# Kernel tuning notes

Measured on AMD Instinct MI355X. Metric: run time of the kernel, lower is better.

## Reference

```python
import jax, jax.numpy as jnp
import numpy as np
from jax import lax

MEM_SLOTS = 100
DECAY = 0.9


def setup_inputs() -> dict:
    key = jax.random.key(0)
    k1, k2, k3 = jax.random.split(key, 3)
    feats = jax.random.normal(k1, (32, 512, 64, 64), dtype=jnp.float32)
    preds = jax.random.uniform(k2, (32, 1, 64, 64), dtype=jnp.float32)
    W = jax.random.normal(k3, (256, 512), dtype=jnp.float32) * 0.02
    b = jnp.zeros((256,), dtype=jnp.float32)
    return {"feats": feats, "preds": preds, "W": W, "b": b, "epoch": 20}


def _update_memory(pooled, threshold):
    """Sequential codebook update: cosine-sim match -> EMA update or append.
    pooled: [B, C]. Returns (memory [100, C], ptr int32)."""
    C = pooled.shape[1]
    slot_ids = jnp.arange(MEM_SLOTS)

    def step(carry, x):
        memory, ptr = carry
        xn = x / jnp.linalg.norm(x)
        norms = jnp.linalg.norm(memory, axis=-1, keepdims=True)
        mem_n = memory / jnp.where(norms == 0, 1.0, norms)
        sims = mem_n @ xn                                   # [100]
        sims = jnp.where(slot_ids < ptr, sims, -jnp.inf)
        idx = jnp.argmax(sims)
        val = sims[idx]
        do_ema = (ptr > 0) & (val >= threshold)
        ema_mem = memory.at[idx].set(memory[idx] * DECAY + (1.0 - DECAY) * x)
        app_mem = memory.at[ptr].set(x)
        new_mem = jnp.where(do_ema, ema_mem, app_mem)
        new_ptr = jnp.where(do_ema, ptr, ptr + 1)
        return (new_mem, new_ptr), None

    init = (jnp.zeros((MEM_SLOTS, C), pooled.dtype), jnp.int32(0))
    (memory, ptr), _ = lax.scan(step, init, pooled)
    return memory, ptr


def reference(feats, preds, W, b, epoch):
    # 1x1 conv projection 512 -> 256
    proj = jnp.einsum('oc,bchw->bohw', W, feats) + b[None, :, None, None]
    B, C, H, Wd = proj.shape
    HW = H * Wd

    # dynamic threshold (epoch % 10 == 0 in original schedule)
    threshold = (epoch / 10 - 2) * 0.4 / 13 + 0.3

    # masked average pooling (no-grad path in original)
    pooled = jnp.mean(lax.stop_gradient(proj).reshape(B, C, HW)
                      * preds.reshape(B, 1, HW), axis=-1)   # [B, C]
    memory, ptr = _update_memory(pooled, threshold)
    memory = lax.stop_gradient(memory)                      # buffer, no grad

    # memory cross-attention over valid slots only
    key_ = proj.reshape(B, C, HW)
    logit = jnp.einsum('pc,bcl->bpl', memory, key_)         # [B, 100, HW]
    valid = (jnp.arange(MEM_SLOTS) < ptr)[None, :, None]
    logit = jnp.where(valid, logit, -jnp.inf)
    attn = jax.nn.softmax(logit, axis=1)                    # softmax over slots
    aug = jnp.einsum('bpl,pc->bcl', attn, memory).reshape(B, C, H, Wd)
    return jnp.concatenate([proj, aug], axis=1)             # [B, 512, H, W]
```

## Files before the change

### kernel.cpp

```cpp
#include <hip/hip_runtime.h>
#include <math.h>

#define CH_IN   512
#define CH_OUT  256
#define HWD     4096
#define BATCH   32
#define MAXSLOT 32

typedef __attribute__((ext_vector_type(8))) short short8;
typedef __attribute__((ext_vector_type(4))) float floatx4;

__device__ __forceinline__ unsigned int pk_bf16(float a, float b) {
    unsigned int ua = __float_as_uint(a);
    ua += 0x7fffu + ((ua >> 16) & 1u);
    unsigned int ub = __float_as_uint(b);
    ub += 0x7fffu + ((ub >> 16) & 1u);
    return (ua >> 16) | (ub & 0xffff0000u);
}

#define PA 40
#define PB 42
__global__ __launch_bounds__(256) void k1_proj_gemm(
    const float* __restrict__ feats, const float* __restrict__ preds,
    const float* __restrict__ W, const float* __restrict__ bias,
    float* __restrict__ out, float* __restrict__ pooled)
{
    __shared__ __align__(16) unsigned short As[128 * PA];
    __shared__ __align__(16) unsigned short Bs[128 * PB];

    const int t  = threadIdx.x;
    const int bid  = blockIdx.x;
    const int xcd  = bid & 7;
    const int slot = bid >> 3;
    const int tile = xcd * 128 + (slot >> 1);
    const int ot   = slot & 1;
    const int lt   = tile & 31;
    const int b    = tile >> 5;

    const int l0 = lt * 128, o0 = ot * 128;
    const int lane = t & 63, wid = t >> 6;
    const int wm = wid & 1, wn = wid >> 1;
    const int ln = lane & 15, quad = lane >> 4;

    floatx4 acc[4][4];
    #pragma unroll
    for (int i = 0; i < 4; i++)
        #pragma unroll
        for (int j = 0; j < 4; j++) acc[i][j] = (floatx4){0.f, 0.f, 0.f, 0.f};

    const float* Wb = W + (size_t)o0 * CH_IN;
    const float* Fb = feats + (size_t)b * CH_IN * HWD + l0;

    const int oA = t >> 3, c4 = t & 7;
    const int l4 = t & 31;
    const int cg = t >> 5;

    float4 wst[4], fst[4];
    #pragma unroll
    for (int q = 0; q < 4; q++)
        wst[q] = *(const float4*)(Wb + (size_t)(oA + 32 * q) * CH_IN + c4 * 4);
    #pragma unroll
    for (int j = 0; j < 4; j++)
        fst[j] = *(const float4*)(Fb + (size_t)(cg * 4 + j) * HWD + l4 * 4);

    #pragma unroll 1
    for (int k0 = 0; k0 < CH_IN; k0 += 32) {
        #pragma unroll
        for (int q = 0; q < 4; q++) {
            unsigned int u0 = pk_bf16(wst[q].x, wst[q].y);
            unsigned int u1 = pk_bf16(wst[q].z, wst[q].w);
            *(uint2*)(As + (oA + 32 * q) * PA + c4 * 4) = make_uint2(u0, u1);
        }
        {
            const float v0[4] = {fst[0].x, fst[0].y, fst[0].z, fst[0].w};
            const float v1[4] = {fst[1].x, fst[1].y, fst[1].z, fst[1].w};
            const float v2[4] = {fst[2].x, fst[2].y, fst[2].z, fst[2].w};
            const float v3[4] = {fst[3].x, fst[3].y, fst[3].z, fst[3].w};
            #pragma unroll
            for (int i = 0; i < 4; i++) {
                unsigned short* row = Bs + (l4 * 4 + i) * PB + cg * 4;
                *(unsigned int*)(row)     = pk_bf16(v0[i], v1[i]);
                *(unsigned int*)(row + 2) = pk_bf16(v2[i], v3[i]);
            }
        }
        __syncthreads();

        if (k0 + 32 < CH_IN) {
            #pragma unroll
            for (int q = 0; q < 4; q++)
                wst[q] = *(const float4*)(Wb + (size_t)(oA + 32 * q) * CH_IN
                                          + (k0 + 32) + c4 * 4);
            #pragma unroll
            for (int j = 0; j < 4; j++)
                fst[j] = *(const float4*)(Fb + (size_t)(k0 + 32 + cg * 4 + j) * HWD
                                          + l4 * 4);
        }

        short8 af[4], bf[4];
        #pragma unroll
        for (int mt = 0; mt < 4; mt++) {
            int row = wm * 64 + mt * 16 + ln;
            af[mt] = *(const short8*)(As + row * PA + quad * 8);
        }
        #pragma unroll
        for (int nt = 0; nt < 4; nt++) {
            int row = wn * 64 + nt * 16 + ln;
            const unsigned short* p = Bs + row * PB + quad * 8;
            union { short8 v; unsigned int u[4]; } r;
            r.u[0] = *(const unsigned int*)(p);
            r.u[1] = *(const unsigned int*)(p + 2);
            r.u[2] = *(const unsigned int*)(p + 4);
            r.u[3] = *(const unsigned int*)(p + 6);
            bf[nt] = r.v;
        }
        #pragma unroll
        for (int mt = 0; mt < 4; mt++)
            #pragma unroll
            for (int nt = 0; nt < 4; nt++)
                acc[mt][nt] = __builtin_amdgcn_mfma_f32_16x16x32_bf16(
                    af[mt], bf[nt], acc[mt][nt], 0, 0, 0);
        __syncthreads();
    }

    float pv[4];
    #pragma unroll
    for (int nt = 0; nt < 4; nt++)
        pv[nt] = preds[(size_t)b * HWD + l0 + wn * 64 + nt * 16 + ln];

    #pragma unroll
    for (int mt = 0; mt < 4; mt++) {
        #pragma unroll
        for (int r = 0; r < 4; r++) {
            int o = o0 + wm * 64 + mt * 16 + quad * 4 + r;
            float bv = bias[o];
            float* op = out + ((size_t)b * 512 + o) * HWD + l0 + wn * 64;
            float psum = 0.f;
            #pragma unroll
            for (int nt = 0; nt < 4; nt++) {
                float val = acc[mt][nt][r] + bv;
                op[nt * 16 + ln] = val;
                psum += val * pv[nt];
            }
            #pragma unroll
            for (int off = 1; off < 16; off <<= 1)
                psum += __shfl_xor(psum, off, 64);
            if (ln == 0)
                atomicAdd(&pooled[(size_t)b * CH_OUT + o], psum);
        }
    }
}

__global__ __launch_bounds__(1024) void k2_mem_update(
    const float* __restrict__ pooled, const int* __restrict__ epoch_p,
    float* __restrict__ mem_out, int* __restrict__ ptr_out)
{
    __shared__ float mem[MAXSLOT][256];
    __shared__ float xs[256];
    __shared__ float norms2[MAXSLOT];
    __shared__ float sims[MAXSLOT];
    __shared__ float red[4];
    __shared__ float xnorm2_s;
    __shared__ int ptr_s, row_s, ema_s;

    const int t = threadIdx.x;
    const int lane = t & 63, wid = t >> 6;

    if (t < 256)
        for (int r = 0; r < MAXSLOT; r++) mem[r][t] = 0.f;
    if (t < MAXSLOT) norms2[t] = 0.f;
    if (t == 0) ptr_s = 0;

    double thr_d = ((double)(*epoch_p)) / 10.0 - 2.0;
    thr_d = thr_d * 0.4 / 13.0 + 0.3;
    const float thr = (float)thr_d;
    __syncthreads();

    for (int bi = 0; bi < BATCH; bi++) {
        if (t < 256) {
            float x = pooled[(size_t)bi * 256 + t] * (1.0f / 4096.0f);
            xs[t] = x;
            float s = x * x;
            #pragma unroll
            for (int off = 32; off >= 1; off >>= 1) s += __shfl_xor(s, off, 64);
            if (lane == 0) red[wid] = s;
        }
        __syncthreads();
        if (t == 0) xnorm2_s = red[0] + red[1] + red[2] + red[3];
        __syncthreads();

        const int P = ptr_s;
        const float xn = sqrtf(xnorm2_s);
        for (int p = wid; p < P; p += 16) {
            float d = mem[p][lane]       * xs[lane]
                    + mem[p][lane + 64]  * xs[lane + 64]
                    + mem[p][lane + 128] * xs[lane + 128]
                    + mem[p][lane + 192] * xs[lane + 192];
            #pragma unroll
            for (int off = 32; off >= 1; off >>= 1) d += __shfl_xor(d, off, 64);
            if (lane == 0) {
                float nrm = sqrtf(norms2[p]);
                if (nrm == 0.f) nrm = 1.f;
                sims[p] = d / (nrm * xn);
            }
        }
        __syncthreads();

        if (wid == 0) {
            float v = (lane < P) ? sims[lane] : -INFINITY;
            int idx = lane;
            #pragma unroll
            for (int off = 32; off >= 1; off >>= 1) {
                float ov = __shfl_down(v, off, 64);
                int   oi = __shfl_down(idx, off, 64);
                if (ov > v || (ov == v && oi < idx)) { v = ov; idx = oi; }
            }
            if (lane == 0) {
                int ema = (P > 0 && v >= thr) ? 1 : 0;
                ema_s = ema;
                row_s = ema ? idx : P;
                if (!ema) ptr_s = P + 1;
            }
        }
        __syncthreads();

        const int r = row_s;
        if (t < 256) {
            float nv = ema_s ? (mem[r][t] * 0.9f + 0.1f * xs[t]) : xs[t];
            mem[r][t] = nv;
            float s2 = nv * nv;
            #pragma unroll
            for (int off = 32; off >= 1; off >>= 1) s2 += __shfl_xor(s2, off, 64);
            if (lane == 0) red[wid] = s2;
        }
        __syncthreads();
        if (t == 0) norms2[r] = red[0] + red[1] + red[2] + red[3];
        __syncthreads();
    }

    if (t < 256)
        for (int r = 0; r < MAXSLOT; r++) mem_out[(size_t)r * 256 + t] = mem[r][t];
    if (t == 0) ptr_out[0] = ptr_s;
}

#define PT  132
#define PMS 40
#define PBS 42
__global__ __launch_bounds__(256) void k3_attention(
    const float* __restrict__ mem_g, const int* __restrict__ ptr_g,
    float* __restrict__ out)
{
    __shared__ __align__(16) unsigned short memS[10240];
    __shared__ __align__(16) unsigned short Bs[128 * PBS];
    __shared__ __align__(16) float attnL[MAXSLOT * PT];

    const int t = threadIdx.x;
    const int lt = blockIdx.x, b = blockIdx.y;
    const int l0 = lt * 128;
    const int P = ptr_g[0];

    const int lane = t & 63, wid = t >> 6;
    const int wm = wid & 1, wn = wid >> 1;
    const int ln = lane & 15, quad = lane >> 4;

    #pragma unroll
    for (int q = 0; q < 16; q++) {
        int idx = t + 256 * q;
        int p = idx >> 7, cp = idx & 127;
        float2 v = *(const float2*)(mem_g + (size_t)p * 256 + cp * 2);
        *(unsigned int*)(memS + (cp >> 4) * (32 * PMS) + p * PMS + (cp & 15) * 2)
            = pk_bf16(v.x, v.y);
    }

    const float* Pb = out + (size_t)b * 512 * HWD + l0;
    const int l4 = t & 31;
    const int cg = t >> 5;

    floatx4 accA[4];
    #pragma unroll
    for (int nt = 0; nt < 4; nt++) accA[nt] = (floatx4){0.f, 0.f, 0.f, 0.f};

    for (int k0 = 0; k0 < 8; k0++) {
        float4 f0 = *(const float4*)(Pb + (size_t)(k0 * 32 + cg * 4 + 0) * HWD + l4 * 4);
        float4 f1 = *(const float4*)(Pb + (size_t)(k0 * 32 + cg * 4 + 1) * HWD + l4 * 4);
        float4 f2 = *(const float4*)(Pb + (size_t)(k0 * 32 + cg * 4 + 2) * HWD + l4 * 4);
        float4 f3 = *(const float4*)(Pb + (size_t)(k0 * 32 + cg * 4 + 3) * HWD + l4 * 4);
        {
            const float v0[4] = {f0.x, f0.y, f0.z, f0.w};
            const float v1[4] = {f1.x, f1.y, f1.z, f1.w};
            const float v2[4] = {f2.x, f2.y, f2.z, f2.w};
            const float v3[4] = {f3.x, f3.y, f3.z, f3.w};
            #pragma unroll
            for (int i = 0; i < 4; i++) {
                unsigned short* row = Bs + (l4 * 4 + i) * PBS + cg * 4;
                *(unsigned int*)(row)     = pk_bf16(v0[i], v1[i]);
                *(unsigned int*)(row + 2) = pk_bf16(v2[i], v3[i]);
            }
        }
        __syncthreads();

        short8 af = *(const short8*)(memS + k0 * (32 * PMS) + (wm * 16 + ln) * PMS + quad * 8);
        short8 bf[4];
        #pragma unroll
        for (int nt = 0; nt < 4; nt++) {
            const unsigned short* p = Bs + (wn * 64 + nt * 16 + ln) * PBS + quad * 8;
            union { short8 v; unsigned int u[4]; } r;
            r.u[0] = *(const unsigned int*)(p);
            r.u[1] = *(const unsigned int*)(p + 2);
            r.u[2] = *(const unsigned int*)(p + 4);
            r.u[3] = *(const unsigned int*)(p + 6);
            bf[nt] = r.v;
        }
        #pragma unroll
        for (int nt = 0; nt < 4; nt++)
            accA[nt] = __builtin_amdgcn_mfma_f32_16x16x32_bf16(af, bf[nt], accA[nt], 0, 0, 0);
        __syncthreads();
    }

    #pragma unroll
    for (int nt = 0; nt < 4; nt++)
        #pragma unroll
        for (int r = 0; r < 4; r++)
            attnL[(wm * 16 + quad * 4 + r) * PT + wn * 64 + nt * 16 + ln] = accA[nt][r];
    __syncthreads();

    if (t < 128) {
        float m = -INFINITY;
        for (int p = 0; p < P; p++) m = fmaxf(m, attnL[p * PT + t]);
        float d = 0.f;
        for (int p = 0; p < P; p++) {
            float e = __expf(attnL[p * PT + t] - m);
            attnL[p * PT + t] = e;
            d += e;
        }
        float inv = 1.f / d;
        for (int p = 0; p < P; p++) attnL[p * PT + t] *= inv;
    }
    __syncthreads();

    if (t < 128) {
        #pragma unroll
        for (int pp = 0; pp < 16; pp++) {
            float a = (2 * pp     < P) ? attnL[(2 * pp) * PT + t]     : 0.f;
            float c = (2 * pp + 1 < P) ? attnL[(2 * pp + 1) * PT + t] : 0.f;
            *(unsigned int*)(Bs + t * PBS + pp * 2) = pk_bf16(a, c);
        }
    }
    #pragma unroll
    for (int q = 0; q < 16; q++) {
        int idx = t + 256 * q;
        int c = idx & 255, pp = idx >> 8;
        float va = mem_g[(size_t)(2 * pp)     * 256 + c];
        float vb = mem_g[(size_t)(2 * pp + 1) * 256 + c];
        *(unsigned int*)(memS + c * PMS + pp * 2) = pk_bf16(va, vb);
    }
    __syncthreads();

    short8 bfc[4];
    #pragma unroll
    for (int nt = 0; nt < 4; nt++) {
        const unsigned short* p = Bs + (wn * 64 + nt * 16 + ln) * PBS + quad * 8;
        union { short8 v; unsigned int u[4]; } r;
        r.u[0] = *(const unsigned int*)(p);
        r.u[1] = *(const unsigned int*)(p + 2);
        r.u[2] = *(const unsigned int*)(p + 4);
        r.u[3] = *(const unsigned int*)(p + 6);
        bfc[nt] = r.v;
    }
    const floatx4 zf = (floatx4){0.f, 0.f, 0.f, 0.f};
    for (int h = 0; h < 2; h++) {
        const int cbase = h * 128 + wm * 64;
        short8 afc[4];
        #pragma unroll
        for (int ct = 0; ct < 4; ct++)
            afc[ct] = *(const short8*)(memS + (cbase + ct * 16 + ln) * PMS + quad * 8);
        #pragma unroll
        for (int ct = 0; ct < 4; ct++) {
            floatx4 accC[4];
            #pragma unroll
            for (int nt = 0; nt < 4; nt++)
                accC[nt] = __builtin_amdgcn_mfma_f32_16x16x32_bf16(afc[ct], bfc[nt], zf, 0, 0, 0);
            #pragma unroll
            for (int r = 0; r < 4; r++) {
                int c = cbase + ct * 16 + quad * 4 + r;
                float* op = out + ((size_t)b * 512 + 256 + c) * HWD + l0 + wn * 64;
                #pragma unroll
                for (int nt = 0; nt < 4; nt++)
                    op[nt * 16 + ln] = accC[nt][r];
            }
        }
    }
}

extern "C" void kernel_launch(void* const* d_in, const int* in_sizes, int n_in,
                              void* d_out, int out_size, void* d_ws, size_t ws_size,
                              hipStream_t stream) {
    const float* feats = (const float*)d_in[0];
    const float* preds = (const float*)d_in[1];
    const float* W     = (const float*)d_in[2];
    const float* bias  = (const float*)d_in[3];
    const int*   epoch = (const int*)d_in[4];
    float* out = (float*)d_out;

    float* ws     = (float*)d_ws;
    float* pooled = ws;
    float* mem_g  = ws + 8192;
    int*   ptr_g  = (int*)(ws + 16384);

    hipMemsetAsync(pooled, 0, 8192 * sizeof(float), stream);

    k1_proj_gemm<<<dim3(2048), 256, 0, stream>>>(feats, preds, W, bias, out, pooled);
    k2_mem_update<<<1, 1024, 0, stream>>>(pooled, epoch, mem_g, ptr_g);
    k3_attention<<<dim3(32, 32), 256, 0, stream>>>(mem_g, ptr_g, out);
}
```

Measured before the change: 600.9 us.

## Rewrite memory-update kernel as single-wavefront loop without block barriers

The sequential codebook update kernel now runs on one 64-lane wavefront instead of 1024 threads. All pooled vectors are prefetched into LDS up front, and the per-step reductions, argmax and broadcast use wave shuffles, which removes the several __syncthreads per batch step. Each pair of lanes computes one slot's dot product with float4 LDS reads, with padded rows to avoid bank conflicts. This relies on implicit wavefront lockstep for the LDS writes and reads between phases, and the kernel is a small part of total time next to the GEMM and attention kernels.

```diff
diff --git a/kernel.cpp b/kernel.cpp
--- a/kernel.cpp
+++ b/kernel.cpp
@@ -150,96 +150,108 @@
     }
 }
 
-__global__ __launch_bounds__(1024) void k2_mem_update(
+#define PMEM 260
+__global__ __launch_bounds__(64) void k2_mem_update(
     const float* __restrict__ pooled, const int* __restrict__ epoch_p,
     float* __restrict__ mem_out, int* __restrict__ ptr_out)
 {
-    __shared__ float mem[MAXSLOT][256];
-    __shared__ float xs[256];
+    __shared__ __align__(16) float memL[MAXSLOT * PMEM];
+    __shared__ __align__(16) float xsAll[BATCH * PMEM];
     __shared__ float norms2[MAXSLOT];
-    __shared__ float sims[MAXSLOT];
-    __shared__ float red[4];
-    __shared__ float xnorm2_s;
-    __shared__ int ptr_s, row_s, ema_s;
-
-    const int t = threadIdx.x;
-    const int lane = t & 63, wid = t >> 6;
-
-    if (t < 256)
-        for (int r = 0; r < MAXSLOT; r++) mem[r][t] = 0.f;
-    if (t < MAXSLOT) norms2[t] = 0.f;
-    if (t == 0) ptr_s = 0;
+    __shared__ float simsL[MAXSLOT];
+
+    const int l = threadIdx.x;
+
+    for (int i = l; i < MAXSLOT * PMEM; i += 64) memL[i] = 0.f;
+    if (l < MAXSLOT) norms2[l] = 0.f;
+
+    #pragma unroll 1
+    for (int j = 0; j < BATCH; j++) {
+        float4 v = *(const float4*)(pooled + (size_t)j * 256 + l * 4);
+        float* dst = xsAll + j * PMEM + l * 4;
+        dst[0] = v.x * (1.0f / 4096.0f);
+        dst[1] = v.y * (1.0f / 4096.0f);
+        dst[2] = v.z * (1.0f / 4096.0f);
+        dst[3] = v.w * (1.0f / 4096.0f);
+    }
 
     double thr_d = ((double)(*epoch_p)) / 10.0 - 2.0;
     thr_d = thr_d * 0.4 / 13.0 + 0.3;
     const float thr = (float)thr_d;
-    __syncthreads();
-
+
+    const int sp = l >> 1, half = l & 1;
+    int ptr = 0;
+
+    #pragma unroll 1
     for (int bi = 0; bi < BATCH; bi++) {
-        if (t < 256) {
-            float x = pooled[(size_t)bi * 256 + t] * (1.0f / 4096.0f);
-            xs[t] = x;
-            float s = x * x;
-            #pragma unroll
-            for (int off = 32; off >= 1; off >>= 1) s += __shfl_xor(s, off, 64);
-            if (lane == 0) red[wid] = s;
-        }
-        __syncthreads();
-        if (t == 0) xnorm2_s = red[0] + red[1] + red[2] + red[3];
-        __syncthreads();
-
-        const int P = ptr_s;
-        const float xn = sqrtf(xnorm2_s);
-        for (int p = wid; p < P; p += 16) {
-            float d = mem[p][lane]       * xs[lane]
-                    + mem[p][lane + 64]  * xs[lane + 64]
-                    + mem[p][lane + 128] * xs[lane + 128]
-                    + mem[p][lane + 192] * xs[lane + 192];
-            #pragma unroll
-            for (int off = 32; off >= 1; off >>= 1) d += __shfl_xor(d, off, 64);
-            if (lane == 0) {
-                float nrm = sqrtf(norms2[p]);
+        const float* xs = xsAll + bi * PMEM;
+
+        float s = xs[l] * xs[l] + xs[l + 64] * xs[l + 64]
+                + xs[l + 128] * xs[l + 128] + xs[l + 192] * xs[l + 192];
+        #pragma unroll
+        for (int off = 32; off >= 1; off >>= 1) s += __shfl_xor(s, off, 64);
+        const float xn = sqrtf(s);
+
+        const int P = ptr;
+
+        {
+            const float* mrow = memL + sp * PMEM + half * 128;
+            const float* xrow = xs + half * 128;
+            float d = 0.f;
+            #pragma unroll
+            for (int i = 0; i < 32; i++) {
+                float4 m  = *(const float4*)(mrow + i * 4);
+                float4 xv = *(const float4*)(xrow + i * 4);
+                d = fmaf(m.x, xv.x, d);
+                d = fmaf(m.y, xv.y, d);
+                d = fmaf(m.z, xv.z, d);
+                d = fmaf(m.w, xv.w, d);
+            }
+            d += __shfl_xor(d, 1, 64);
+            if (half == 0) {
+                float nrm = sqrtf(norms2[sp]);
                 if (nrm == 0.f) nrm = 1.f;
-                sims[p] = d / (nrm * xn);
-            }
-        }
-        __syncthreads();
-
-        if (wid == 0) {
-            float v = (lane < P) ? sims[lane] : -INFINITY;
-            int idx = lane;
-            #pragma unroll
-            for (int off = 32; off >= 1; off >>= 1) {
-                float ov = __shfl_down(v, off, 64);
-                int   oi = __shfl_down(idx, off, 64);
-                if (ov > v || (ov == v && oi < idx)) { v = ov; idx = oi; }
-            }
-            if (lane == 0) {
-                int ema = (P > 0 && v >= thr) ? 1 : 0;
-                ema_s = ema;
-                row_s = ema ? idx : P;
-                if (!ema) ptr_s = P + 1;
-            }
-        }
-        __syncthreads();
-
-        const int r = row_s;
-        if (t < 256) {
-            float nv = ema_s ? (mem[r][t] * 0.9f + 0.1f * xs[t]) : xs[t];
-            mem[r][t] = nv;
-            float s2 = nv * nv;
-            #pragma unroll
-            for (int off = 32; off >= 1; off >>= 1) s2 += __shfl_xor(s2, off, 64);
-            if (lane == 0) red[wid] = s2;
-        }
-        __syncthreads();
-        if (t == 0) norms2[r] = red[0] + red[1] + red[2] + red[3];
-        __syncthreads();
-    }
-
-    if (t < 256)
-        for (int r = 0; r < MAXSLOT; r++) mem_out[(size_t)r * 256 + t] = mem[r][t];
-    if (t == 0) ptr_out[0] = ptr_s;
+                simsL[sp] = d / (nrm * xn);
+            }
+        }
+
+        float v = (l < P) ? simsL[l] : -INFINITY;
+        int idx = l;
+        #pragma unroll
+        for (int off = 32; off >= 1; off >>= 1) {
+            float ov = __shfl_down(v, off, 64);
+            int   oi = __shfl_down(idx, off, 64);
+            if (ov > v || (ov == v && oi < idx)) { v = ov; idx = oi; }
+        }
+        int ema = 0, row = 0;
+        if (l == 0) {
+            ema = (P > 0 && v >= thr) ? 1 : 0;
+            row = ema ? idx : P;
+        }
+        ema = __shfl(ema, 0, 64);
+        row = __shfl(row, 0, 64);
+        if (!ema) ptr = P + 1;
+
+        float* mr = memL + row * PMEM;
+        float s2 = 0.f;
+        #pragma unroll
+        for (int k = 0; k < 4; k++) {
+            int c = l + 64 * k;
+            float nv = ema ? (mr[c] * 0.9f + 0.1f * xs[c]) : xs[c];
+            mr[c] = nv;
+            s2 = fmaf(nv, nv, s2);
+        }
+        #pragma unroll
+        for (int off = 32; off >= 1; off >>= 1) s2 += __shfl_xor(s2, off, 64);
+        if (l == 0) norms2[row] = s2;
+    }
+
+    #pragma unroll 1
+    for (int r = 0; r < MAXSLOT; r++) {
+        float4 v = *(const float4*)(memL + r * PMEM + l * 4);
+        *(float4*)(mem_out + (size_t)r * 256 + l * 4) = v;
+    }
+    if (l == 0) ptr_out[0] = ptr;
 }
 
 #define PT  132
@@ -409,6 +421,6 @@
     hipMemsetAsync(pooled, 0, 8192 * sizeof(float), stream);
 
     k1_proj_gemm<<<dim3(2048), 256, 0, stream>>>(feats, preds, W, bias, out, pooled);
-    k2_mem_update<<<1, 1024, 0, stream>>>(pooled, epoch, mem_g, ptr_g);
+    k2_mem_update<<<1, 64, 0, stream>>>(pooled, epoch, mem_g, ptr_g);
     k3_attention<<<dim3(32, 32), 256, 0, stream>>>(mem_g, ptr_g, out);
 }
```

Result: faster. 586.8 us (-2.4%).
